# Kernel tuning notes

Hardware: AMD Instinct MI355X
Metric: run time of the kernel (lower is better)

The kernel has to match this reference:

```python
import jax, jax.numpy as jnp
import numpy as np

TEMPERATURE = 0.2
HYPER_GAMMA = 0.5
EPS = 1e-12  # torch F.normalize / cosine_similarity eps guard (1e-12 / 1e-8)

def setup_inputs() -> dict:
    key = jax.random.key(0)
    k1, k2 = jax.random.split(key)
    B, D = 4096, 1024
    return {
        "emb_i": jax.random.normal(k1, (B, D), dtype=jnp.float32),
        "emb_j": jax.random.normal(k2, (B, D), dtype=jnp.float32),
    }

def _l2_normalize(x, eps=EPS):
    n = jnp.sqrt(jnp.sum(x * x, axis=1, keepdims=True))
    return x / jnp.maximum(n, eps)

def reference(emb_i, emb_j):
    B = emb_i.shape[0]
    z_i = _l2_normalize(emb_i)
    z_j = _l2_normalize(emb_j)
    # cosine similarity of unit vectors == dot product; sim[a, b] = <z_j[a], z_i[b]>
    sim = jnp.einsum('ad,bd->ab', z_j, z_i)  # [B, B]
    sim_positive = jnp.diagonal(sim)
    positives_exp = jnp.exp(-sim_positive + TEMPERATURE)
    neg_mask = 1.0 - jnp.eye(B, dtype=sim.dtype)
    negatives_exp = neg_mask * jnp.exp(sim - TEMPERATURE)
    positives_sum = jnp.sum(jnp.log1p(positives_exp)) / B
    negatives_sum = jnp.sum(jnp.log1p(negatives_exp)) / (B * (B - 1))
    return HYPER_GAMMA * positives_sum + (1.0 - HYPER_GAMMA) * negatives_sum
```

## Files before the change

### kernel.cpp

```cpp
#include <hip/hip_runtime.h>
#include <math.h>

#define B_ROWS 4096
#define D_DIM  1024
static constexpr float TEMP = 0.2f;
static constexpr float FP8_SCALE = 16.0f;
static constexpr float INV_S2 = 1.0f / 256.0f;

typedef __attribute__((ext_vector_type(4)))  int   i32x4;
typedef __attribute__((ext_vector_type(8)))  int   i32x8;
typedef __attribute__((ext_vector_type(4)))  float f32x4;

__device__ inline unsigned char f2fp8(float f) {
    unsigned int u = __float_as_uint(f);
    unsigned int s = (u >> 24) & 0x80u;
    float af = fabsf(f);
    unsigned char b;
    if (af >= 0x1.0p-6f) {
        unsigned int au = u & 0x7fffffffu;
        unsigned int lsb = (au >> 20) & 1u;
        au += 0x7ffffu + lsb;
        int e = (int)(au >> 23) - 127 + 7;
        unsigned int m = (au >> 20) & 7u;
        if (e > 15 || (e == 15 && m > 6)) b = 0x7e;
        else b = (unsigned char)((e << 3) | m);
    } else {
        int q = (int)rintf(af * 512.0f);
        b = (unsigned char)(q >= 8 ? 0x08 : q);
    }
    return (unsigned char)(b | s);
}

__device__ inline unsigned int f2fp8x4(float4 v) {
    return (unsigned int)f2fp8(v.x)
         | ((unsigned int)f2fp8(v.y) << 8)
         | ((unsigned int)f2fp8(v.z) << 16)
         | ((unsigned int)f2fp8(v.w) << 24);
}

__device__ inline void gload_lds16(const unsigned char* g, unsigned char* l) {
    __builtin_amdgcn_global_load_lds(
        (const __attribute__((address_space(1))) unsigned int*)g,
        (__attribute__((address_space(3))) unsigned int*)l,
        16, 0, 0);
}

__device__ inline i32x8 read_frag(const unsigned char* p, int o0, int o1) {
    i32x4 lo = *(const i32x4*)(p + o0);
    i32x4 hi = *(const i32x4*)(p + o1);
    return __builtin_shufflevector(lo, hi, 0, 1, 2, 3, 4, 5, 6, 7);
}

#define MX_MFMA(A, Bv, C) __builtin_amdgcn_mfma_scale_f32_16x16x128_f8f6f4( \
    (A), (Bv), (C), 0, 0, 0, 0x7f7f7f7f, 0, 0x7f7f7f7f)


__global__ __launch_bounds__(256) void norm_cast_kernel(
        const float* __restrict__ emb_i, const float* __restrict__ emb_j,
        unsigned char* __restrict__ Zi8, unsigned char* __restrict__ Zj8,
        float* __restrict__ w) {
    const int tid = threadIdx.x;
    if (blockIdx.x == 0 && tid == 0) {
        w[0] = 0.0f; w[1] = 0.0f;
        ((unsigned int*)w)[2] = 0u;
    }
    const int wave = tid >> 6, lane = tid & 63;
    const int row = blockIdx.x * 4 + wave;
    const float* src; unsigned char* dst; int r;
    if (row < B_ROWS) { src = emb_i; dst = Zi8; r = row; }
    else              { src = emb_j; dst = Zj8; r = row - B_ROWS; }

    const float4* p = (const float4*)(src + (size_t)r * D_DIM);
    float4 v0 = p[lane], v1 = p[64 + lane], v2 = p[128 + lane], v3 = p[192 + lane];
    float s = v0.x*v0.x + v0.y*v0.y + v0.z*v0.z + v0.w*v0.w
            + v1.x*v1.x + v1.y*v1.y + v1.z*v1.z + v1.w*v1.w
            + v2.x*v2.x + v2.y*v2.y + v2.z*v2.z + v2.w*v2.w
            + v3.x*v3.x + v3.y*v3.y + v3.z*v3.z + v3.w*v3.w;
    #pragma unroll
    for (int m = 1; m < 64; m <<= 1) s += __shfl_xor(s, m, 64);
    const float inv = FP8_SCALE / fmaxf(sqrtf(s), 1e-12f);

    float4 a0 = {v0.x*inv, v0.y*inv, v0.z*inv, v0.w*inv};
    float4 a1 = {v1.x*inv, v1.y*inv, v1.z*inv, v1.w*inv};
    float4 a2 = {v2.x*inv, v2.y*inv, v2.z*inv, v2.w*inv};
    float4 a3 = {v3.x*inv, v3.y*inv, v3.z*inv, v3.w*inv};
    unsigned int* q = (unsigned int*)(dst + (size_t)r * D_DIM);
    q[lane]       = f2fp8x4(a0);
    q[64 + lane]  = f2fp8x4(a1);
    q[128 + lane] = f2fp8x4(a2);
    q[192 + lane] = f2fp8x4(a3);
}

__global__ __launch_bounds__(256) void simloss_mfma_mxfp8_kernel(
        const unsigned char* __restrict__ Zi8,
        const unsigned char* __restrict__ Zj8,
        float* __restrict__ w, float* __restrict__ out) {
    __shared__ __align__(16) unsigned char lA[128 * 128];
    __shared__ __align__(16) unsigned char lB[128 * 128];
    __shared__ float rn[4], rp[4];

    const int tid  = threadIdx.x;
    const int lane = tid & 63;
    const int wave = tid >> 6;
    const int wy = wave >> 1, wx = wave & 1;
    const int rowBase = blockIdx.y * 128;
    const int colBase = blockIdx.x * 128;

    const int srow = lane >> 3;
    const int sc   = (lane & 7) ^ srow;
    const unsigned char* gA = Zj8 + (size_t)(rowBase + 32*wave + srow) * D_DIM + sc*16;
    const unsigned char* gB = Zi8 + (size_t)(colBase + 32*wave + srow) * D_DIM + sc*16;
    unsigned char* sA = lA + wave * 4096;
    unsigned char* sB = lB + wave * 4096;

    const int lr16 = lane & 15;
    const int g    = lane >> 4;
    const int o0 = ((((g << 1) + 0) ^ (lane & 7)) << 4);
    const int o1 = ((((g << 1) + 1) ^ (lane & 7)) << 4);
    const unsigned char* fA = lA + (wy * 64 + lr16) * 128;
    const unsigned char* fB = lB + (wx * 64 + lr16) * 128;

    f32x4 acc[4][4];
    #pragma unroll
    for (int i = 0; i < 4; ++i)
        #pragma unroll
        for (int j = 0; j < 4; ++j)
            acc[i][j] = (f32x4){0.f, 0.f, 0.f, 0.f};

    for (int it = 0; it < 8; ++it) {
        __syncthreads();
        const int k0 = it * 128;
        #pragma unroll
        for (int n = 0; n < 4; ++n) {
            gload_lds16(gA + (size_t)(n*8) * D_DIM + k0, sA + n*1024);
            gload_lds16(gB + (size_t)(n*8) * D_DIM + k0, sB + n*1024);
        }
        __syncthreads();

        i32x8 a0 = read_frag(fA,        o0, o1);
        i32x8 a1 = read_frag(fA + 2048, o0, o1);
        i32x8 a2 = read_frag(fA + 4096, o0, o1);
        i32x8 a3 = read_frag(fA + 6144, o0, o1);
        i32x8 b0 = read_frag(fB,        o0, o1);
        i32x8 b1 = read_frag(fB + 2048, o0, o1);
        i32x8 b2 = read_frag(fB + 4096, o0, o1);
        i32x8 b3 = read_frag(fB + 6144, o0, o1);
        acc[0][0] = MX_MFMA(a0, b0, acc[0][0]);
        acc[0][1] = MX_MFMA(a0, b1, acc[0][1]);
        acc[0][2] = MX_MFMA(a0, b2, acc[0][2]);
        acc[0][3] = MX_MFMA(a0, b3, acc[0][3]);
        acc[1][0] = MX_MFMA(a1, b0, acc[1][0]);
        acc[1][1] = MX_MFMA(a1, b1, acc[1][1]);
        acc[1][2] = MX_MFMA(a1, b2, acc[1][2]);
        acc[1][3] = MX_MFMA(a1, b3, acc[1][3]);
        acc[2][0] = MX_MFMA(a2, b0, acc[2][0]);
        acc[2][1] = MX_MFMA(a2, b1, acc[2][1]);
        acc[2][2] = MX_MFMA(a2, b2, acc[2][2]);
        acc[2][3] = MX_MFMA(a2, b3, acc[2][3]);
        acc[3][0] = MX_MFMA(a3, b0, acc[3][0]);
        acc[3][1] = MX_MFMA(a3, b1, acc[3][1]);
        acc[3][2] = MX_MFMA(a3, b2, acc[3][2]);
        acc[3][3] = MX_MFMA(a3, b3, acc[3][3]);
    }

    float neg = 0.f, pos = 0.f;
    const int bc = colBase + wx * 64 + lr16;
    #pragma unroll
    for (int i = 0; i < 4; ++i) {
        const int abase = rowBase + wy * 64 + i * 16 + g * 4;
        #pragma unroll
        for (int j = 0; j < 4; ++j) {
            const int b = bc + j * 16;
            #pragma unroll
            for (int r = 0; r < 4; ++r) {
                const float x = acc[i][j][r] * INV_S2 - TEMP;
                if (abase + r == b) pos += __logf(1.0f + __expf(-x));
                else                neg += __logf(1.0f + __expf(x));
            }
        }
    }
    #pragma unroll
    for (int o = 32; o > 0; o >>= 1) {
        neg += __shfl_down(neg, o, 64);
        pos += __shfl_down(pos, o, 64);
    }
    if (lane == 0) { rn[wave] = neg; rp[wave] = pos; }
    __syncthreads();
    if (tid == 0) {
        atomicAdd(&w[1], rn[0] + rn[1] + rn[2] + rn[3]);
        if (blockIdx.x == blockIdx.y)
            atomicAdd(&w[0], rp[0] + rp[1] + rp[2] + rp[3]);
        __threadfence();
        unsigned int done = atomicAdd(((unsigned int*)w) + 2, 1u);
        if (done == gridDim.x * gridDim.y - 1) {
            const float psum = atomicAdd(&w[0], 0.0f);
            const float nsum = atomicAdd(&w[1], 0.0f);
            out[0] = 0.5f * (psum / (float)B_ROWS)
                   + 0.5f * (nsum / ((float)B_ROWS * (float)(B_ROWS - 1)));
        }
    }
}

extern "C" void kernel_launch(void* const* d_in, const int* in_sizes, int n_in,
                              void* d_out, int out_size, void* d_ws, size_t ws_size,
                              hipStream_t stream) {
    const float* emb_i = (const float*)d_in[0];
    const float* emb_j = (const float*)d_in[1];
    float* w = (float*)d_ws;
    unsigned char* Zi8 = (unsigned char*)(w + 16);
    unsigned char* Zj8 = Zi8 + (size_t)B_ROWS * D_DIM;
    float* out = (float*)d_out;

    norm_cast_kernel<<<2 * B_ROWS / 4, 256, 0, stream>>>(emb_i, emb_j, Zi8, Zj8, w);
    dim3 grid(B_ROWS / 128, B_ROWS / 128);
    simloss_mfma_mxfp8_kernel<<<grid, 256, 0, stream>>>(Zi8, Zj8, w, out);
}
```

Before: 130.4 us.

## Double-buffer LDS tiles to overlap global loads with MFMA compute

Splits shared memory into two 32KB stages and prefetches the next K-slice with global_load_lds while computing on the current one, replacing the two barriers per iteration with one. This aims to hide global-to-LDS latency behind the MFMA work. LDS use doubles to 64KB per block, which may lower occupancy. Correctness relies on __syncthreads draining the asynchronous LDS loads (vmcnt) before the buffer is read.

```diff
diff --git a/kernel.cpp b/kernel.cpp
--- a/kernel.cpp
+++ b/kernel.cpp
@@ -95,8 +95,7 @@
         const unsigned char* __restrict__ Zi8,
         const unsigned char* __restrict__ Zj8,
         float* __restrict__ w, float* __restrict__ out) {
-    __shared__ __align__(16) unsigned char lA[128 * 128];
-    __shared__ __align__(16) unsigned char lB[128 * 128];
+    __shared__ __align__(16) unsigned char lds[2 * 32768];
     __shared__ float rn[4], rp[4];
 
     const int tid  = threadIdx.x;
@@ -110,15 +109,25 @@
     const int sc   = (lane & 7) ^ srow;
     const unsigned char* gA = Zj8 + (size_t)(rowBase + 32*wave + srow) * D_DIM + sc*16;
     const unsigned char* gB = Zi8 + (size_t)(colBase + 32*wave + srow) * D_DIM + sc*16;
-    unsigned char* sA = lA + wave * 4096;
-    unsigned char* sB = lB + wave * 4096;
+    const int sAoff = wave * 4096;
+    const int sBoff = 16384 + wave * 4096;
+
+#define STAGE(k0, bo) do {                                                     \
+        _Pragma("unroll")                                                      \
+        for (int n = 0; n < 4; ++n) {                                          \
+            gload_lds16(gA + (size_t)(n*8) * D_DIM + (k0),                     \
+                        lds + (bo) + sAoff + n*1024);                          \
+            gload_lds16(gB + (size_t)(n*8) * D_DIM + (k0),                     \
+                        lds + (bo) + sBoff + n*1024);                          \
+        }                                                                      \
+    } while (0)
 
     const int lr16 = lane & 15;
     const int g    = lane >> 4;
     const int o0 = ((((g << 1) + 0) ^ (lane & 7)) << 4);
     const int o1 = ((((g << 1) + 1) ^ (lane & 7)) << 4);
-    const unsigned char* fA = lA + (wy * 64 + lr16) * 128;
-    const unsigned char* fB = lB + (wx * 64 + lr16) * 128;
+    const int fAoff = (wy * 64 + lr16) * 128;
+    const int fBoff = 16384 + (wx * 64 + lr16) * 128;
 
     f32x4 acc[4][4];
     #pragma unroll
@@ -127,16 +136,14 @@
         for (int j = 0; j < 4; ++j)
             acc[i][j] = (f32x4){0.f, 0.f, 0.f, 0.f};
 
+    STAGE(0, 0);
+    __syncthreads();
+    int cur = 0;
     for (int it = 0; it < 8; ++it) {
-        __syncthreads();
-        const int k0 = it * 128;
-        #pragma unroll
-        for (int n = 0; n < 4; ++n) {
-            gload_lds16(gA + (size_t)(n*8) * D_DIM + k0, sA + n*1024);
-            gload_lds16(gB + (size_t)(n*8) * D_DIM + k0, sB + n*1024);
-        }
-        __syncthreads();
-
+        if (it < 7) STAGE((it + 1) * 128, cur ^ 32768);
+
+        const unsigned char* fA = lds + cur + fAoff;
+        const unsigned char* fB = lds + cur + fBoff;
         i32x8 a0 = read_frag(fA,        o0, o1);
         i32x8 a1 = read_frag(fA + 2048, o0, o1);
         i32x8 a2 = read_frag(fA + 4096, o0, o1);
@@ -161,7 +168,11 @@
         acc[3][1] = MX_MFMA(a3, b1, acc[3][1]);
         acc[3][2] = MX_MFMA(a3, b2, acc[3][2]);
         acc[3][3] = MX_MFMA(a3, b3, acc[3][3]);
-    }
+
+        __syncthreads();
+        cur ^= 32768;
+    }
+#undef STAGE
 
     float neg = 0.f, pos = 0.f;
     const int bc = colBase + wx * 64 + lr16;
```

Result: slower. 155.6 us (+19.3%).
